# Kernel optimization log

Hardware: AMD Instinct MI355X
Metric: run time of the kernel (lower is better)

The kernel has to match this reference:

```python
import jax, jax.numpy as jnp
import numpy as np

B, IN_SHAPE, EXP_SHAPE, HID, NB_CLASSES = 64, 10000, 53, 1500, 2048


def setup_inputs() -> dict:
    key = jax.random.key(0)
    ks = jax.random.split(key, 8)
    gos = jax.random.uniform(ks[0], (B, IN_SHAPE), dtype=jnp.float32)
    exp_x = jax.random.uniform(ks[1], (B, EXP_SHAPE), dtype=jnp.float32)
    # FlatModel params (torch Linear: y = x @ W.T + b; store pre-transposed)
    W1 = jax.random.normal(ks[2], (IN_SHAPE, HID), dtype=jnp.float32) * (1.0 / np.sqrt(IN_SHAPE))
    b1 = jnp.zeros((HID,), dtype=jnp.float32)
    W2 = jax.random.normal(ks[3], (HID + EXP_SHAPE, NB_CLASSES), dtype=jnp.float32) * (1.0 / np.sqrt(HID + EXP_SHAPE))
    b2 = jnp.zeros((NB_CLASSES,), dtype=jnp.float32)
    # HPO adjacency (non-trainable buffer in the original; values in [0,1))
    hpo_matrix = jax.random.uniform(ks[4], (NB_CLASSES, NB_CLASSES), dtype=jnp.float32)
    return {"gos": gos, "exp_x": exp_x, "W1": W1, "b1": b1, "W2": W2, "b2": b2, "hpo_matrix": hpo_matrix}


def reference(gos, exp_x, W1, b1, W2, b2, hpo_matrix):
    # FlatModel (eval mode: dropout is identity). torch F.gelu default = exact erf gelu.
    h = jax.nn.gelu(gos @ W1 + b1, approximate=False)          # (B, HID)
    x = jnp.concatenate([h, exp_x], axis=1)                     # (B, HID+EXP)
    flat = jax.nn.sigmoid(x @ W2 + b2)                          # (B, C)
    # HPOLayer + permute + MaxPool1d(C): out[b,j] = max_i flat[b,j] * M[i,j]
    out = jnp.max(flat[:, None, :] * hpo_matrix[None, :, :], axis=1)  # (B, C)
    return out
```

## Files before the change

### kernel.cpp

```cpp
#include <hip/hip_runtime.h>
#include <math.h>


#define B64 64
#define IN_SH 10000
#define EXP_SH 53
#define HID 1500
#define NPAD1 1536
#define NBC 2048
#define K2 1553
#define KS1 20
#define KST1 16
#define KST2 52
#define CMCH 32
#define ACC1 (NPAD1 * 64)

using short8  = __attribute__((ext_vector_type(8))) short;
using floatx4 = __attribute__((ext_vector_type(4))) float;
using uintx4  = __attribute__((ext_vector_type(4))) unsigned int;

__device__ __forceinline__ unsigned short f2bf(float f) {
    unsigned u = __float_as_uint(f);
    u += 0x7fffu + ((u >> 16) & 1u);
    return (unsigned short)(u >> 16);
}

typedef __attribute__((address_space(3))) void lds_v;
typedef __attribute__((address_space(1))) const void glb_v;
__device__ __forceinline__ void gll16(const float* g, float* l) {
    __builtin_amdgcn_global_load_lds((glb_v*)g, (lds_v*)l, 16, 0, 0);
}

#define WVS(n) asm volatile("s_waitcnt vmcnt(" #n ")" ::: "memory")
template<int N> __device__ __forceinline__ void waitv() {
    if constexpr (N >= 44)      WVS(44);
    else if constexpr (N >= 40) WVS(40);
    else if constexpr (N >= 36) WVS(36);
    else if constexpr (N >= 32) WVS(32);
    else if constexpr (N >= 28) WVS(28);
    else if constexpr (N >= 24) WVS(24);
    else if constexpr (N >= 20) WVS(20);
    else if constexpr (N >= 16) WVS(16);
    else if constexpr (N >= 12) WVS(12);
    else if constexpr (N >= 10) WVS(10);
    else if constexpr (N >= 8)  WVS(8);
    else if constexpr (N >= 6)  WVS(6);
    else if constexpr (N >= 4)  WVS(4);
    else if constexpr (N >= 2)  WVS(2);
    else                        WVS(0);
}

constexpr int after_ops(int KS, int RING, int st) {
    int n = 0;
    if (st < RING) {
        n += 2 * (RING - 1 - st) + 8;
        for (int k = 0; k < st; k++)
            n += (k + RING < KS ? 2 : 0) + (k + 2 < KS ? 4 : 0);
    } else {
        n += (st - RING + 2 < KS ? 4 : 0);
        for (int k = st - RING + 1; k < st; k++)
            n += (k + RING < KS ? 2 : 0) + (k + 2 < KS ? 4 : 0);
    }
    return n;
}

template<int KS, int RING, int ST>
__device__ __forceinline__ void gstep(
    const float* __restrict__ W, const unsigned short* __restrict__ bf,
    float* __restrict__ ldsw, floatx4 (&acc)[4], uintx4 (&bv)[3][4],
    unsigned wbase, unsigned stepInc, unsigned halfInc, unsigned maxoff,
    int q, int l15)
{
    if constexpr (ST < KS) {
        constexpr int AO = after_ops(KS, RING, ST);
        waitv<(AO > 6 ? AO - 6 : 0)>();
        const float* lb = ldsw + (ST % RING) * 512;
        short8 af;
        #pragma unroll
        for (int j = 0; j < 8; j++)
            af[j] = (short)f2bf(lb[(q * 8 + j) * 16 + l15]);
        if constexpr (ST + RING < KS) {
            unsigned o0 = wbase + (unsigned)(ST + RING) * stepInc;
            unsigned o1 = o0 + halfInc;
            if (o0 > maxoff) o0 = maxoff;
            if (o1 > maxoff) o1 = maxoff;
            gll16(W + o0, ldsw + ((ST + RING) % RING) * 512);
            gll16(W + o1, ldsw + ((ST + RING) % RING) * 512 + 256);
        }
        if constexpr (ST + 2 < KS) {
            #pragma unroll
            for (int s = 0; s < 4; s++)
                bv[(ST + 2) % 3][s] =
                    *(const uintx4*)(bf + (size_t)((ST + 2) * 4 + s) * 512);
        }
        #pragma unroll
        for (int s = 0; s < 4; s++) {
            short8 b8 = __builtin_bit_cast(short8, bv[ST % 3][s]);
            acc[s] = __builtin_amdgcn_mfma_f32_16x16x32_bf16(af, b8, acc[s], 0, 0, 0);
        }
        gstep<KS, RING, ST + 1>(W, bf, ldsw, acc, bv, wbase, stepInc, halfInc,
                                maxoff, q, l15);
    }
}

template<int KS, int RING>
__device__ __forceinline__ void gemm_ring(
    const float* __restrict__ W, const unsigned short* __restrict__ Bfc,
    floatx4 (&acc)[4], int ldw, unsigned maxoff, int n0, int k0,
    int lane, float* __restrict__ ldsw)
{
    const int q = lane >> 4, l15 = lane & 15;
    const int r = lane >> 2, c4 = (lane & 3) * 4;
    unsigned wbase = (unsigned)((k0 + r) * ldw + n0 + c4);
    const unsigned stepInc = 32u * (unsigned)ldw;
    const unsigned halfInc = 16u * (unsigned)ldw;

    #pragma unroll
    for (int st = 0; st < RING; st++) {
        unsigned o0 = wbase + (unsigned)st * stepInc;
        unsigned o1 = o0 + halfInc;
        if (o0 > maxoff) o0 = maxoff;
        if (o1 > maxoff) o1 = maxoff;
        gll16(W + o0, ldsw + st * 512);
        gll16(W + o1, ldsw + st * 512 + 256);
    }
    const unsigned short* bf = Bfc + (size_t)lane * 8;
    uintx4 bv[3][4];
    #pragma unroll
    for (int k = 0; k < 2; k++) {
        #pragma unroll
        for (int s = 0; s < 4; s++)
            bv[k][s] = *(const uintx4*)(bf + (size_t)(k * 4 + s) * 512);
    }
    #pragma unroll
    for (int s = 0; s < 4; s++) acc[s] = (floatx4){0.f, 0.f, 0.f, 0.f};

    gstep<KS, RING, 0>(W, bf, ldsw, acc, bv, wbase, stepInc, halfInc, maxoff, q, l15);
}

__global__ __launch_bounds__(256) void prep_k(
    const float* __restrict__ g, unsigned short* __restrict__ gosBf,
    const float* __restrict__ M, float* __restrict__ cm)
{
    int bi = blockIdx.x;
    if (bi < 320) {
        int t    = bi * 256 + threadIdx.x;
        int lane = t & 63;
        int sgrp = (t >> 6) & 3;
        int step = t >> 8;
        int q    = lane >> 4;
        int l15  = lane & 15;
        int b    = sgrp * 16 + l15;
        int k0   = step * 32 + q * 8;
        const float* p = g + (size_t)b * IN_SH + k0;
        unsigned int o[4];
        #pragma unroll
        for (int i = 0; i < 4; i++) {
            float lo = (k0 + 2 * i     < IN_SH) ? p[2 * i]     : 0.f;
            float hi = (k0 + 2 * i + 1 < IN_SH) ? p[2 * i + 1] : 0.f;
            o[i] = (unsigned)f2bf(lo) | ((unsigned)f2bf(hi) << 16);
        }
        uintx4 v; v.x = o[0]; v.y = o[1]; v.z = o[2]; v.w = o[3];
        *(uintx4*)(gosBf + (size_t)t * 8) = v;
    } else {
        int u  = bi - 320;
        int j  = (u & 7) * 256 + threadIdx.x;
        int i0 = (u >> 3) * 64;
        float m = 0.0f;
        #pragma unroll 16
        for (int i = i0; i < i0 + 64; i++)
            m = fmaxf(m, M[(size_t)i * NBC + j]);
        cm[(u >> 3) * NBC + j] = m;
    }
}

__global__ __launch_bounds__(256, 4) void gemm1_k(
    const float* __restrict__ W1, const unsigned short* __restrict__ gosBf,
    float* __restrict__ hpre_p)
{
    __shared__ float lds[4 * 2048];
    int bi  = blockIdx.x;
    int swz = (bi & 7) * 60 + (bi >> 3);
    int bx  = swz % 24;
    int by  = swz / 24;
    int wid = threadIdx.x >> 6;
    int lane = threadIdx.x & 63;
    floatx4 acc[4];
    gemm_ring<KST1, 4>(W1, gosBf + (size_t)by * (KST1 * 4) * 512, acc, HID,
                       (unsigned)(IN_SH * HID - 4),
                       bx * 64 + wid * 16, by * (KST1 * 32),
                       lane, lds + wid * 2048);
    int q = lane >> 4, l15 = lane & 15;
    int nrow = bx * 64 + wid * 16 + q * 4;
    float* pbuf = hpre_p + (size_t)by * ACC1;
    #pragma unroll
    for (int s = 0; s < 4; s++) {
        #pragma unroll
        for (int rr = 0; rr < 4; rr++)
            pbuf[(size_t)(nrow + rr) * 64 + s * 16 + l15] = acc[s][rr];
    }
}

__global__ __launch_bounds__(256) void combine1(
    const float* __restrict__ hpre_p, const float* __restrict__ b1,
    const float* __restrict__ expx, unsigned short* __restrict__ Xf,
    const float* __restrict__ cm, float* __restrict__ cmr)
{
    int bi = blockIdx.x;
    if (bi < 208) {
        int idx = bi * 256 + threadIdx.x;
        int b   = idx & 63;
        int n0  = (idx >> 6) * 2;
        float v[2];
        #pragma unroll
        for (int e = 0; e < 2; e++) {
            int n = n0 + e;
            float x = 0.f;
            if (n < HID) {
                const float* p = hpre_p + (size_t)n * 64 + b;
                float a0 = 0.f, a1 = 0.f, a2 = 0.f, a3 = 0.f;
                #pragma unroll
                for (int ks = 0; ks < KS1; ks += 4) {
                    a0 += p[(size_t)ks * ACC1];
                    a1 += p[(size_t)(ks + 1) * ACC1];
                    a2 += p[(size_t)(ks + 2) * ACC1];
                    a3 += p[(size_t)(ks + 3) * ACC1];
                }
                float s = b1[n] + ((a0 + a1) + (a2 + a3));
                x = 0.5f * s * (1.0f + erff(s * 0.70710678118654752f));
            } else if (n < HID + EXP_SH) {
                x = expx[b * EXP_SH + (n - HID)];
            }
            v[e] = x;
        }
        unsigned o = (unsigned)f2bf(v[0]) | ((unsigned)f2bf(v[1]) << 16);
        int step = n0 >> 5, w = n0 & 31, q = w >> 3, j = w & 7;
        int sgrp = b >> 4, l15 = b & 15;
        size_t tq = (size_t)(step * 4 + sgrp) * 64 + q * 16 + l15;
        *(unsigned*)(Xf + tq * 8 + j) = o;
    } else {
        int j = (bi - 208) * 256 + threadIdx.x;
        float m = 0.f;
        #pragma unroll
        for (int c = 0; c < CMCH; c++) m = fmaxf(m, cm[c * NBC + j]);
        cmr[j] = m;
    }
}

__global__ __launch_bounds__(256) void gemm2_k(
    const float* __restrict__ W2, const unsigned short* __restrict__ Xf,
    const float* __restrict__ b2, const float* __restrict__ cmr,
    float* __restrict__ out)
{
    __shared__ float lds[4 * 4096];
    int tid = threadIdx.x, lane = tid & 63, wid = tid >> 6;
    int j0 = blockIdx.x * 64;
    int n0 = j0 + wid * 16;
    floatx4 acc[4];
    gemm_ring<KST2, 8>(W2, Xf, acc, NBC, (unsigned)(K2 * NBC - 4),
                       n0, 0, lane, lds + wid * 4096);
    int q = lane >> 4, l15 = lane & 15;
    __syncthreads();
    #pragma unroll
    for (int s = 0; s < 4; s++) {
        #pragma unroll
        for (int rr = 0; rr < 4; rr++) {
            int j = n0 + q * 4 + rr;
            float v = acc[s][rr] + b2[j];
            v = (1.0f / (1.0f + expf(-v))) * cmr[j];
            lds[(wid * 16 + q * 4 + rr) * 65 + s * 16 + l15] = v;
        }
    }
    __syncthreads();
    #pragma unroll
    for (int e = 0; e < 16; e++) {
        int lin = e * 256 + tid;
        int b   = lin >> 6;
        int jj  = lin & 63;
        out[(size_t)b * NBC + j0 + jj] = lds[jj * 65 + b];
    }
}

extern "C" void kernel_launch(void* const* d_in, const int* in_sizes, int n_in,
                              void* d_out, int out_size, void* d_ws, size_t ws_size,
                              hipStream_t stream) {
    const float* gos  = (const float*)d_in[0];
    const float* expx = (const float*)d_in[1];
    const float* W1   = (const float*)d_in[2];
    const float* b1   = (const float*)d_in[3];
    const float* W2   = (const float*)d_in[4];
    const float* b2   = (const float*)d_in[5];
    const float* hpo  = (const float*)d_in[6];
    float* out = (float*)d_out;

    char* ws = (char*)d_ws;
    unsigned short* gosBf = (unsigned short*)ws;
    unsigned short* Xf    = (unsigned short*)(ws + 1310720);
    float* cm     = (float*)(ws + 1523712);
    float* cmr    = (float*)(ws + 1785856);
    float* hpre_p = (float*)(ws + 1794048);

    prep_k<<<576, 256, 0, stream>>>(gos, gosBf, hpo, cm);

    gemm1_k<<<480, 256, 0, stream>>>(W1, gosBf, hpre_p);

    combine1<<<216, 256, 0, stream>>>(hpre_p, b1, expx, Xf, cm, cmr);

    gemm2_k<<<32, 256, 0, stream>>>(W2, Xf, b2, cmr, out);
}
```

Measured before the change: 174.1 us.

## Split GEMM2 K dimension across waves and launch more blocks

The second GEMM goes from 32 blocks, each with four waves covering different 16-column slices over the full K range, to 128 blocks that each own one 16-column slice. The four waves in a block split K into quarters and their partial sums are reduced through LDS before bias, sigmoid and the max-factor are applied. The aim is to fill more CUs on a GEMM that was badly under-parallelised. The cost is an intra-block reduction and a shallower pipeline per wave, whose ring depth drops from 8 to 4.

```diff
diff --git a/kernel.cpp b/kernel.cpp
--- a/kernel.cpp
+++ b/kernel.cpp
@@ -11,7 +11,7 @@
 #define K2 1553
 #define KS1 20
 #define KST1 16
-#define KST2 52
+#define KC2 13
 #define CMCH 32
 #define ACC1 (NPAD1 * 64)
 
@@ -247,38 +247,40 @@
     }
 }
 
-__global__ __launch_bounds__(256) void gemm2_k(
+__global__ __launch_bounds__(256) void gemm2f_k(
     const float* __restrict__ W2, const unsigned short* __restrict__ Xf,
     const float* __restrict__ b2, const float* __restrict__ cmr,
     float* __restrict__ out)
 {
-    __shared__ float lds[4 * 4096];
+    __shared__ float lds[4 * 2048];
     int tid = threadIdx.x, lane = tid & 63, wid = tid >> 6;
-    int j0 = blockIdx.x * 64;
-    int n0 = j0 + wid * 16;
+    int bi  = blockIdx.x;
+    int n0  = ((bi & 7) * 16 + (bi >> 3)) * 16;
     floatx4 acc[4];
-    gemm_ring<KST2, 8>(W2, Xf, acc, NBC, (unsigned)(K2 * NBC - 4),
-                       n0, 0, lane, lds + wid * 4096);
-    int q = lane >> 4, l15 = lane & 15;
+    gemm_ring<KC2, 4>(W2, Xf + (size_t)(wid * KC2 * 4) * 512, acc, NBC,
+                      (unsigned)(K2 * NBC - 4), n0, wid * KC2 * 32,
+                      lane, lds + wid * 2048);
     __syncthreads();
     #pragma unroll
     for (int s = 0; s < 4; s++) {
         #pragma unroll
-        for (int rr = 0; rr < 4; rr++) {
-            int j = n0 + q * 4 + rr;
-            float v = acc[s][rr] + b2[j];
-            v = (1.0f / (1.0f + expf(-v))) * cmr[j];
-            lds[(wid * 16 + q * 4 + rr) * 65 + s * 16 + l15] = v;
-        }
+        for (int rr = 0; rr < 4; rr++)
+            lds[wid * 1024 + lane * 16 + s * 4 + rr] = acc[s][rr];
     }
     __syncthreads();
-    #pragma unroll
-    for (int e = 0; e < 16; e++) {
-        int lin = e * 256 + tid;
-        int b   = lin >> 6;
-        int jj  = lin & 63;
-        out[(size_t)b * NBC + j0 + jj] = lds[jj * 65 + b];
-    }
+    int b = tid >> 2, j4 = (tid & 3) * 4;
+    int s = b >> 4, l15 = b & 15;
+    floatx4 v;
+    #pragma unroll
+    for (int e = 0; e < 4; e++) {
+        int j = j4 + e;
+        int q = j >> 2, rr = j & 3;
+        int flat = (q * 16 + l15) * 16 + s * 4 + rr;
+        float x = lds[flat] + lds[1024 + flat] + lds[2048 + flat] + lds[3072 + flat];
+        x += b2[n0 + j];
+        v[e] = (1.0f / (1.0f + expf(-x))) * cmr[n0 + j];
+    }
+    *(floatx4*)(out + (size_t)b * NBC + n0 + j4) = v;
 }
 
 extern "C" void kernel_launch(void* const* d_in, const int* in_sizes, int n_in,
@@ -306,5 +308,5 @@
 
     combine1<<<216, 256, 0, stream>>>(hpre_p, b1, expx, Xf, cm, cmr);
 
-    gemm2_k<<<32, 256, 0, stream>>>(W2, Xf, b2, cmr, out);
-}
+    gemm2f_k<<<128, 256, 0, stream>>>(W2, Xf, b2, cmr, out);
+}
```

Result: faster. 159.0 us (-8.6%).

## Split-K the second GEMM across blocks and add a reduction epilogue kernel

Applied to the files above, without the earlier changes.

The second GEMM now launches a 2D grid that splits the K dimension into 13 chunks, each block writing partial logits to workspace. A new final kernel sums the partials, adds bias, applies sigmoid and the column-max scale, and transposes to the output. This raises parallelism from 32 blocks to many more on a large GPU, at the cost of extra partial-sum traffic and one more kernel launch.

```diff
diff --git a/kernel.cpp b/kernel.cpp
--- a/kernel.cpp
+++ b/kernel.cpp
@@ -11,9 +11,11 @@
 #define K2 1553
 #define KS1 20
 #define KST1 16
-#define KST2 52
+#define KS2 13
+#define KST2 4
 #define CMCH 32
 #define ACC1 (NPAD1 * 64)
+#define ACC2 (NBC * 64)
 
 using short8  = __attribute__((ext_vector_type(8))) short;
 using floatx4 = __attribute__((ext_vector_type(4))) float;
@@ -247,36 +249,56 @@
     }
 }
 
-__global__ __launch_bounds__(256) void gemm2_k(
+__global__ __launch_bounds__(256, 4) void gemm2_k(
     const float* __restrict__ W2, const unsigned short* __restrict__ Xf,
-    const float* __restrict__ b2, const float* __restrict__ cmr,
-    float* __restrict__ out)
-{
-    __shared__ float lds[4 * 4096];
-    int tid = threadIdx.x, lane = tid & 63, wid = tid >> 6;
-    int j0 = blockIdx.x * 64;
-    int n0 = j0 + wid * 16;
+    float* __restrict__ logits_p)
+{
+    __shared__ float lds[4 * 2048];
+    int wid = threadIdx.x >> 6;
+    int lane = threadIdx.x & 63;
+    int n0 = blockIdx.x * 64 + wid * 16;
     floatx4 acc[4];
-    gemm_ring<KST2, 8>(W2, Xf, acc, NBC, (unsigned)(K2 * NBC - 4),
-                       n0, 0, lane, lds + wid * 4096);
+    gemm_ring<KST2, 4>(W2, Xf + (size_t)blockIdx.y * (KST2 * 4) * 512, acc,
+                       NBC, (unsigned)(K2 * NBC - 4),
+                       n0, blockIdx.y * (KST2 * 32), lane, lds + wid * 2048);
     int q = lane >> 4, l15 = lane & 15;
+    int nrow = n0 + q * 4;
+    float* pbuf = logits_p + (size_t)blockIdx.y * ACC2;
+    #pragma unroll
+    for (int s = 0; s < 4; s++) {
+        #pragma unroll
+        for (int rr = 0; rr < 4; rr++)
+            pbuf[(size_t)(nrow + rr) * 64 + s * 16 + l15] = acc[s][rr];
+    }
+}
+
+__global__ __launch_bounds__(256) void final_k(
+    const float* __restrict__ logits_p, const float* __restrict__ b2,
+    const float* __restrict__ cmr, float* __restrict__ out)
+{
+    __shared__ float lds[32 * 65];
+    int j0  = blockIdx.x * 32;
+    int tid = threadIdx.x;
+    #pragma unroll
+    for (int e = 0; e < 8; e++) {
+        int lin = e * 256 + tid;
+        int jj  = lin >> 6;
+        int b   = lin & 63;
+        int j   = j0 + jj;
+        float s = b2[j];
+        const float* p = logits_p + (size_t)j * 64 + b;
+        #pragma unroll
+        for (int ks = 0; ks < KS2; ks++)
+            s += p[(size_t)ks * ACC2];
+        float sig = 1.0f / (1.0f + expf(-s));
+        lds[jj * 65 + b] = sig * cmr[j];
+    }
     __syncthreads();
     #pragma unroll
-    for (int s = 0; s < 4; s++) {
-        #pragma unroll
-        for (int rr = 0; rr < 4; rr++) {
-            int j = n0 + q * 4 + rr;
-            float v = acc[s][rr] + b2[j];
-            v = (1.0f / (1.0f + expf(-v))) * cmr[j];
-            lds[(wid * 16 + q * 4 + rr) * 65 + s * 16 + l15] = v;
-        }
-    }
-    __syncthreads();
-    #pragma unroll
-    for (int e = 0; e < 16; e++) {
+    for (int e = 0; e < 8; e++) {
         int lin = e * 256 + tid;
-        int b   = lin >> 6;
-        int jj  = lin & 63;
+        int b   = lin >> 5;
+        int jj  = lin & 31;
         out[(size_t)b * NBC + j0 + jj] = lds[jj * 65 + b];
     }
 }
@@ -296,9 +318,10 @@
     char* ws = (char*)d_ws;
     unsigned short* gosBf = (unsigned short*)ws;
     unsigned short* Xf    = (unsigned short*)(ws + 1310720);
-    float* cm     = (float*)(ws + 1523712);
-    float* cmr    = (float*)(ws + 1785856);
-    float* hpre_p = (float*)(ws + 1794048);
+    float* cm       = (float*)(ws + 1523712);
+    float* cmr      = (float*)(ws + 1785856);
+    float* hpre_p   = (float*)(ws + 1794048);
+    float* logits_p = (float*)(ws + 9658368);
 
     prep_k<<<576, 256, 0, stream>>>(gos, gosBf, hpo, cm);
 
@@ -306,5 +329,7 @@
 
     combine1<<<216, 256, 0, stream>>>(hpre_p, b1, expx, Xf, cm, cmr);
 
-    gemm2_k<<<32, 256, 0, stream>>>(W2, Xf, b2, cmr, out);
-}
+    gemm2_k<<<dim3(32, KS2), 256, 0, stream>>>(W2, Xf, logits_p);
+
+    final_k<<<64, 256, 0, stream>>>(logits_p, b2, cmr, out);
+}
```

After: 158.7 us. 1.1x faster.
